# Kernel tuning notes

Measured on AMD Instinct MI355X. Metric: run time of the kernel, lower is better.

Reference implementation:

```python
import jax, jax.numpy as jnp
import numpy as np

N = 100000          # number of nodes (src == dst in this sampled graph)
DEG = 8             # uniform sampled fan-in (max_num_neighbors)
E = N * DEG         # number of edges
IN_C = 128
HEADS = 4
OUT_C = 32
NEG_SLOPE = 0.2


def setup_inputs() -> dict:
    key = jax.random.key(0)
    k1, k2, k3, k4, k5 = jax.random.split(key, 5)
    x = jax.random.normal(k1, (N, IN_C), dtype=jnp.float32)
    csr_row_ptr = jnp.arange(N + 1, dtype=jnp.int64) * DEG
    csr_col_ind = jax.random.randint(k2, (E,), 0, N, dtype=jnp.int64)
    # learned params (xavier-normal-ish scaling)
    lin_w = jax.random.normal(k3, (IN_C, HEADS * OUT_C), dtype=jnp.float32) * np.sqrt(2.0 / (IN_C + HEADS * OUT_C))
    att = jax.random.normal(k4, (2 * HEADS * OUT_C,), dtype=jnp.float32) * np.sqrt(2.0 / (1 + OUT_C))
    bias = jnp.zeros((HEADS * OUT_C,), dtype=jnp.float32)
    return {"x": x, "csr_row_ptr": csr_row_ptr, "csr_col_ind": csr_col_ind,
            "max_num_neighbors": DEG, "lin_w": lin_w, "att": att, "bias": bias}


def reference(x, csr_row_ptr, csr_col_ind, max_num_neighbors, lin_w, att, bias):
    n = x.shape[0]
    e = csr_col_ind.shape[0]
    hc = HEADS * OUT_C
    # linear projection: [N, H, C]
    xp = (x @ lin_w).reshape(n, HEADS, OUT_C)
    att_src = att[:hc].reshape(HEADS, OUT_C)
    att_dst = att[hc:].reshape(HEADS, OUT_C)
    # per-node attention logits per head: [N, H]
    a_src = jnp.einsum('nhc,hc->nh', xp, att_src)
    a_dst = jnp.einsum('nhc,hc->nh', xp, att_dst)
    # expand CSR row_ptr into per-edge destination ids: [E]
    dst = jnp.searchsorted(csr_row_ptr, jnp.arange(e, dtype=csr_row_ptr.dtype), side='right') - 1
    src = csr_col_ind
    # edge scores + per-destination softmax over incoming edges
    logits = jax.nn.leaky_relu(a_src[src] + a_dst[dst], NEG_SLOPE)  # [E, H]
    m = jax.ops.segment_max(logits, dst, num_segments=n)            # [N, H]
    ex = jnp.exp(logits - m[dst])
    denom = jax.ops.segment_sum(ex, dst, num_segments=n)            # [N, H]
    alpha = ex / denom[dst]                                         # [E, H]
    # weighted aggregation of neighbor features: [N, H, C]
    out = jax.ops.segment_sum(alpha[:, :, None] * xp[src], dst, num_segments=n)
    out = out.reshape(n, hc) + bias  # concat=True
    return out
```

## Files before the change

kernel.cpp:

```cpp
#include <hip/hip_runtime.h>
#include <stdint.h>

#define HEADS 4
#define NEG_SLOPE 0.2f
#define MB 64

typedef _Float16 f16;
typedef f16 f16x8 __attribute__((ext_vector_type(8)));
typedef f16 f16x4 __attribute__((ext_vector_type(4)));
typedef float f32x4 __attribute__((ext_vector_type(4)));
typedef unsigned int u32x4 __attribute__((ext_vector_type(4)));

#define SWZ(row, kb) (((row) << 8) + ((kb) ^ (((row) & 7) << 4)))

__global__ __launch_bounds__(256) void wt_kernel(const float* __restrict__ w,
                                                 f16* __restrict__ wt) {
    __shared__ f16 tl[16][136];
    const int b = blockIdx.x, t = threadIdx.x;
    for (int i = t; i < 2048; i += 256) {
        int k = i >> 4, nl = i & 15;
        tl[nl][k] = (f16)w[k * 128 + b * 16 + nl];
    }
    __syncthreads();
    {
        int nl = t >> 4, kc = t & 15;
        f16x8 v = *(const f16x8*)&tl[nl][kc * 8];
        *(f16x8*)(wt + (b * 16 + nl) * 128 + kc * 8) = v;
    }
}

__global__ __launch_bounds__(256) void gat_proj_mfma(
    const float* __restrict__ x, const f16* __restrict__ wt,
    const float* __restrict__ att, f16* __restrict__ xp,
    float* __restrict__ a_src, float* __restrict__ a_dst, int n) {
    __shared__ unsigned char lds[32768];
    __shared__ float att_l[256];
    const int t = threadIdx.x;
    const int node0 = blockIdx.x * MB;
    const int lane = t & 63;
    const int wv = t >> 6;

    att_l[t] = att[t];

    const int arow = node0 + wv * 16 + (lane & 15);
    const bool rowok = arow < n;
    const float* xr = x + (size_t)arow * 128 + (lane >> 4) * 8;
    f16x8 afr[4];
#pragma unroll
    for (int kt = 0; kt < 4; kt++) {
        float4 a = make_float4(0.f, 0.f, 0.f, 0.f), b = a;
        if (rowok) {
            a = *(const float4*)(xr + kt * 32);
            b = *(const float4*)(xr + kt * 32 + 4);
        }
        f16x8 hv;
        hv[0] = (f16)a.x; hv[1] = (f16)a.y; hv[2] = (f16)a.z; hv[3] = (f16)a.w;
        hv[4] = (f16)b.x; hv[5] = (f16)b.y; hv[6] = (f16)b.z; hv[7] = (f16)b.w;
        afr[kt] = hv;
    }

    for (int i = t; i < 2048; i += 256) {
        int row = i >> 4, kc = i & 15;
        uint4 v = *(const uint4*)(wt + row * 128 + kc * 8);
        *(uint4*)(lds + SWZ(row, kc * 16)) = v;
    }
    __syncthreads();

    f32x4 acc[8];
#pragma unroll
    for (int nf = 0; nf < 8; nf++) acc[nf] = (f32x4){0.f, 0.f, 0.f, 0.f};

#pragma unroll
    for (int kt = 0; kt < 4; kt++) {
        const int kb = kt * 64 + (lane >> 4) * 16;
#pragma unroll
        for (int nf = 0; nf < 8; nf++) {
            f16x8 bfr = *(const f16x8*)(lds + SWZ(nf * 16 + (lane & 15), kb));
            acc[nf] = __builtin_amdgcn_mfma_f32_16x16x32_f16(afr[kt], bfr, acc[nf], 0, 0, 0);
        }
    }

    __syncthreads();
#pragma unroll
    for (int r = 0; r < 4; r++) {
        int row = wv * 16 + (lane >> 4) * 4 + r;
#pragma unroll
        for (int nf = 0; nf < 8; nf++) {
            int col = nf * 16 + (lane & 15);
            *(f16*)(lds + SWZ(row, col * 2)) = (f16)acc[nf][r];
        }
    }
    __syncthreads();

    {
        int row = t >> 2, h = t & 3;
        int grow = node0 + row;
        if (grow < n) {
            float s = 0.f, d = 0.f;
#pragma unroll
            for (int cc = 0; cc < 4; cc++) {
                f16x8 v = *(const f16x8*)(lds + SWZ(row, h * 64 + cc * 16));
#pragma unroll
                for (int j = 0; j < 8; j++) {
                    float xv = (float)v[j];
                    int c = cc * 8 + j;
                    s = fmaf(xv, att_l[h * 32 + c], s);
                    d = fmaf(xv, att_l[128 + h * 32 + c], d);
                }
            }
            a_src[(size_t)grow * HEADS + h] = s;
            a_dst[(size_t)grow * HEADS + h] = d;
        }
    }
    for (int i = t; i < 1024; i += 256) {
        int row = i >> 4, kc = i & 15;
        int grow = node0 + row;
        if (grow < n) {
            u32x4 v = *(const u32x4*)(lds + SWZ(row, kc * 16));
            int slice = kc >> 2;
            *(u32x4*)(xp + ((size_t)slice * n + grow) * 32 + (kc & 3) * 8) = v;
        }
    }
}

__global__ __launch_bounds__(256) void gat_alpha_kernel(
    const float* __restrict__ a_src, const float* __restrict__ a_dst,
    const int* __restrict__ row_ptr, const int* __restrict__ col_ind,
    f16* __restrict__ alpha, int n, int e_total) {
    const int lane = threadIdx.x & 63;
    const int nb = (blockIdx.x * 4 + (threadIdx.x >> 6)) * 8;
    if (nb >= n) return;
    const int j = lane >> 3, e = lane & 7;
    const int node = nb + j;

    int rp = 0;
    if (lane < 9) {
        int idx = nb + lane;
        if (idx > n) idx = n;
        rp = row_ptr[idx];
    }
    bool ok = __all((lane < 9) ? (rp == (nb + lane) * 8) : 1) && (nb + 8 <= n);

    int ci = 0;
    bool valid;
    if (ok) {
        ci = col_ind[nb * 8 + lane];
        valid = true;
    } else {
        int rs = __shfl(rp, j, 64), re = __shfl(rp, j + 1, 64);
        int dg = re - rs;
        if (dg > 8) dg = 8;
        valid = (node < n) && (e < dg);
        if (valid) ci = col_ind[rs + e];
    }

    f32x4 asv = (f32x4){0.f, 0.f, 0.f, 0.f};
    if (valid) asv = *(const f32x4*)(a_src + (size_t)ci * HEADS);
    f32x4 adv = (f32x4){0.f, 0.f, 0.f, 0.f};
    if (node < n) adv = *(const f32x4*)(a_dst + (size_t)node * HEADS);

#pragma unroll
    for (int h = 0; h < HEADS; h++) {
        float z = asv[h] + adv[h];
        z = (z >= 0.f) ? z : NEG_SLOPE * z;
        float v = valid ? z : -1e30f;
        float m = v;
        m = fmaxf(m, __shfl_xor(m, 1, 64));
        m = fmaxf(m, __shfl_xor(m, 2, 64));
        m = fmaxf(m, __shfl_xor(m, 4, 64));
        float ex = valid ? __expf(v - m) : 0.f;
        float ss = ex;
        ss += __shfl_xor(ss, 1, 64);
        ss += __shfl_xor(ss, 2, 64);
        ss += __shfl_xor(ss, 4, 64);
        float al = ex * ((ss > 0.f) ? (1.f / ss) : 0.f);
        if (node < n)
            alpha[(size_t)h * n * 8 + (size_t)node * 8 + e] = (f16)al;
    }
}

__global__ __launch_bounds__(256) void gat_slice_aggr(
    const f16* __restrict__ xp, const f16* __restrict__ alpha,
    const int* __restrict__ row_ptr, const int* __restrict__ col_ind,
    const float* __restrict__ bias, float* __restrict__ out, int n, int e_total) {
    const int slice = blockIdx.x & 3;
    const int chunk = blockIdx.x >> 2;
    const int lane = threadIdx.x & 63;
    const int nb = chunk * 32 + (threadIdx.x >> 6) * 8;
    if (nb >= n) return;

    const f16* xps = xp + (size_t)slice * n * 32;
    const f16* alp = alpha + (size_t)slice * n * 8;
    const int nd = lane >> 3, c = lane & 7;
    const int node = nb + nd;

    int rp = 0;
    if (lane < 9) {
        int idx = nb + lane;
        if (idx > n) idx = n;
        rp = row_ptr[idx];
    }
    int ci = 0;
    {
        long long si = (long long)nb * 8 + lane;
        if (si < e_total) ci = col_ind[si];
    }
    int av = 0;
    if (lane < 32) {
        long long fi = (long long)nb * 8 + lane * 2;
        if (fi + 2 <= (long long)n * 8) av = *(const int*)(alp + fi);
    }
    float4 b4 = *(const float4*)(bias + slice * 32 + c * 4);

    bool ok = __all((lane < 9) ? (rp == (nb + lane) * 8) : 1) && (nb + 8 <= n);

    float a0 = 0.f, a1 = 0.f, a2 = 0.f, a3 = 0.f;
    if (ok) {
#pragma unroll
        for (int e = 0; e < 8; e++) {
            int src = __shfl(ci, nd * 8 + e, 64);
            int au = __shfl(av, (nd * 8 + e) >> 1, 64);
            unsigned short ab = (e & 1) ? (unsigned short)(((unsigned int)au) >> 16)
                                        : (unsigned short)(au & 0xffff);
            float a = (float)(*(const f16*)&ab);
            f16x4 v = *(const f16x4*)(xps + (size_t)src * 32 + c * 4);
            a0 = fmaf(a, (float)v[0], a0);
            a1 = fmaf(a, (float)v[1], a1);
            a2 = fmaf(a, (float)v[2], a2);
            a3 = fmaf(a, (float)v[3], a3);
        }
    } else {
        int rs = __shfl(rp, nd, 64);
        int re = __shfl(rp, nd + 1, 64);
        int dg = re - rs;
        if (dg > 8) dg = 8;
        if (node < n) {
            for (int e = 0; e < dg; e++) {
                int src = col_ind[rs + e];
                unsigned short ab = *(const unsigned short*)(alp + (size_t)node * 8 + e);
                float a = (float)(*(const f16*)&ab);
                f16x4 v = *(const f16x4*)(xps + (size_t)src * 32 + c * 4);
                a0 = fmaf(a, (float)v[0], a0);
                a1 = fmaf(a, (float)v[1], a1);
                a2 = fmaf(a, (float)v[2], a2);
                a3 = fmaf(a, (float)v[3], a3);
            }
        }
    }

    if (node < n) {
        f32x4 o;
        o[0] = a0 + b4.x;
        o[1] = a1 + b4.y;
        o[2] = a2 + b4.z;
        o[3] = a3 + b4.w;
        __builtin_nontemporal_store(o, (f32x4*)(out + (size_t)node * 128 + slice * 32 + c * 4));
    }
}

extern "C" void kernel_launch(void* const* d_in, const int* in_sizes, int n_in,
                              void* d_out, int out_size, void* d_ws, size_t ws_size,
                              hipStream_t stream) {
    const float* x = (const float*)d_in[0];
    const int* row_ptr = (const int*)d_in[1];
    const int* col_ind = (const int*)d_in[2];
    const float* lin_w = (const float*)d_in[4];
    const float* att = (const float*)d_in[5];
    const float* bias = (const float*)d_in[6];
    float* out = (float*)d_out;
    const int n = in_sizes[0] / 128;
    const int e_total = in_sizes[2];

    f16* xp = (f16*)d_ws;
    float* a_src = (float*)((char*)d_ws + (size_t)n * 256);
    float* a_dst = a_src + (size_t)n * HEADS;
    f16* alpha = (f16*)(a_dst + (size_t)n * HEADS);
    f16* wt = alpha + (size_t)n * 32 + 128;

    hipLaunchKernelGGL(wt_kernel, dim3(8), dim3(256), 0, stream, lin_w, wt);
    hipLaunchKernelGGL(gat_proj_mfma, dim3((n + MB - 1) / MB), dim3(256), 0, stream,
                       x, wt, att, xp, a_src, a_dst, n);
    hipLaunchKernelGGL(gat_alpha_kernel, dim3((n + 31) / 32), dim3(256), 0, stream,
                       a_src, a_dst, row_ptr, col_ind, alpha, n, e_total);
    hipLaunchKernelGGL(gat_slice_aggr, dim3(4 * ((n + 31) / 32)), dim3(256), 0, stream,
                       xp, alpha, row_ptr, col_ind, bias, out, n, e_total);
}
```

Baseline: 75.35 us.

## Fuse edge softmax into slice aggregation kernel and drop alpha buffer

Removes the separate alpha kernel. Each aggregation wavefront now computes the leaky-relu logits, segment max and softmax for its own head slice using warp shuffles, reading a_src and a_dst directly. This drops one launch and the alpha write and read round trip through memory. The eight neighbor feature gathers are now issued before the softmax math so they can overlap with it, at the cost of more registers and scattered a_src gathers repeated once per slice.

```diff
diff --git a/kernel.cpp b/kernel.cpp
--- a/kernel.cpp
+++ b/kernel.cpp
@@ -123,15 +123,20 @@
     }
 }
 
-__global__ __launch_bounds__(256) void gat_alpha_kernel(
-    const float* __restrict__ a_src, const float* __restrict__ a_dst,
-    const int* __restrict__ row_ptr, const int* __restrict__ col_ind,
-    f16* __restrict__ alpha, int n, int e_total) {
+__global__ __launch_bounds__(256) void gat_slice_aggr(
+    const f16* __restrict__ xp, const float* __restrict__ a_src,
+    const float* __restrict__ a_dst, const int* __restrict__ row_ptr,
+    const int* __restrict__ col_ind, const float* __restrict__ bias,
+    float* __restrict__ out, int n, int e_total) {
+    const int slice = blockIdx.x & 3;
+    const int chunk = blockIdx.x >> 2;
     const int lane = threadIdx.x & 63;
-    const int nb = (blockIdx.x * 4 + (threadIdx.x >> 6)) * 8;
+    const int nb = chunk * 32 + (threadIdx.x >> 6) * 8;
     if (nb >= n) return;
-    const int j = lane >> 3, e = lane & 7;
-    const int node = nb + j;
+
+    const f16* xps = xp + (size_t)slice * n * 32;
+    const int nd = lane >> 3, x8 = lane & 7;
+    const int node = nb + nd;
 
     int rp = 0;
     if (lane < 9) {
@@ -139,113 +144,55 @@
         if (idx > n) idx = n;
         rp = row_ptr[idx];
     }
-    bool ok = __all((lane < 9) ? (rp == (nb + lane) * 8) : 1) && (nb + 8 <= n);
-
-    int ci = 0;
-    bool valid;
-    if (ok) {
-        ci = col_ind[nb * 8 + lane];
-        valid = true;
-    } else {
-        int rs = __shfl(rp, j, 64), re = __shfl(rp, j + 1, 64);
-        int dg = re - rs;
-        if (dg > 8) dg = 8;
-        valid = (node < n) && (e < dg);
-        if (valid) ci = col_ind[rs + e];
-    }
-
-    f32x4 asv = (f32x4){0.f, 0.f, 0.f, 0.f};
-    if (valid) asv = *(const f32x4*)(a_src + (size_t)ci * HEADS);
-    f32x4 adv = (f32x4){0.f, 0.f, 0.f, 0.f};
-    if (node < n) adv = *(const f32x4*)(a_dst + (size_t)node * HEADS);
-
-#pragma unroll
-    for (int h = 0; h < HEADS; h++) {
-        float z = asv[h] + adv[h];
-        z = (z >= 0.f) ? z : NEG_SLOPE * z;
-        float v = valid ? z : -1e30f;
-        float m = v;
-        m = fmaxf(m, __shfl_xor(m, 1, 64));
-        m = fmaxf(m, __shfl_xor(m, 2, 64));
-        m = fmaxf(m, __shfl_xor(m, 4, 64));
-        float ex = valid ? __expf(v - m) : 0.f;
-        float ss = ex;
-        ss += __shfl_xor(ss, 1, 64);
-        ss += __shfl_xor(ss, 2, 64);
-        ss += __shfl_xor(ss, 4, 64);
-        float al = ex * ((ss > 0.f) ? (1.f / ss) : 0.f);
-        if (node < n)
-            alpha[(size_t)h * n * 8 + (size_t)node * 8 + e] = (f16)al;
-    }
-}
-
-__global__ __launch_bounds__(256) void gat_slice_aggr(
-    const f16* __restrict__ xp, const f16* __restrict__ alpha,
-    const int* __restrict__ row_ptr, const int* __restrict__ col_ind,
-    const float* __restrict__ bias, float* __restrict__ out, int n, int e_total) {
-    const int slice = blockIdx.x & 3;
-    const int chunk = blockIdx.x >> 2;
-    const int lane = threadIdx.x & 63;
-    const int nb = chunk * 32 + (threadIdx.x >> 6) * 8;
-    if (nb >= n) return;
-
-    const f16* xps = xp + (size_t)slice * n * 32;
-    const f16* alp = alpha + (size_t)slice * n * 8;
-    const int nd = lane >> 3, c = lane & 7;
-    const int node = nb + nd;
-
-    int rp = 0;
-    if (lane < 9) {
-        int idx = nb + lane;
-        if (idx > n) idx = n;
-        rp = row_ptr[idx];
-    }
     int ci = 0;
     {
         long long si = (long long)nb * 8 + lane;
         if (si < e_total) ci = col_ind[si];
     }
-    int av = 0;
-    if (lane < 32) {
-        long long fi = (long long)nb * 8 + lane * 2;
-        if (fi + 2 <= (long long)n * 8) av = *(const int*)(alp + fi);
-    }
-    float4 b4 = *(const float4*)(bias + slice * 32 + c * 4);
+    float4 b4 = *(const float4*)(bias + slice * 32 + x8 * 4);
 
     bool ok = __all((lane < 9) ? (rp == (nb + lane) * 8) : 1) && (nb + 8 <= n);
-
-    float a0 = 0.f, a1 = 0.f, a2 = 0.f, a3 = 0.f;
-    if (ok) {
-#pragma unroll
-        for (int e = 0; e < 8; e++) {
-            int src = __shfl(ci, nd * 8 + e, 64);
-            int au = __shfl(av, (nd * 8 + e) >> 1, 64);
-            unsigned short ab = (e & 1) ? (unsigned short)(((unsigned int)au) >> 16)
-                                        : (unsigned short)(au & 0xffff);
-            float a = (float)(*(const f16*)&ab);
-            f16x4 v = *(const f16x4*)(xps + (size_t)src * 32 + c * 4);
-            a0 = fmaf(a, (float)v[0], a0);
-            a1 = fmaf(a, (float)v[1], a1);
-            a2 = fmaf(a, (float)v[2], a2);
-            a3 = fmaf(a, (float)v[3], a3);
-        }
-    } else {
-        int rs = __shfl(rp, nd, 64);
-        int re = __shfl(rp, nd + 1, 64);
+    bool valid = true;
+    if (!ok) {
+        int rs = __shfl(rp, nd, 64), re = __shfl(rp, nd + 1, 64);
         int dg = re - rs;
         if (dg > 8) dg = 8;
-        if (node < n) {
-            for (int e = 0; e < dg; e++) {
-                int src = col_ind[rs + e];
-                unsigned short ab = *(const unsigned short*)(alp + (size_t)node * 8 + e);
-                float a = (float)(*(const f16*)&ab);
-                f16x4 v = *(const f16x4*)(xps + (size_t)src * 32 + c * 4);
-                a0 = fmaf(a, (float)v[0], a0);
-                a1 = fmaf(a, (float)v[1], a1);
-                a2 = fmaf(a, (float)v[2], a2);
-                a3 = fmaf(a, (float)v[3], a3);
-            }
-        }
+        if (node >= n) dg = 0;
+        valid = x8 < dg;
+        ci = valid ? col_ind[rs + x8] : 0;
+    }
+
+    f16x4 pv[8];
+#pragma unroll
+    for (int e = 0; e < 8; e++) {
+        int src = __shfl(ci, nd * 8 + e, 64);
+        pv[e] = *(const f16x4*)(xps + (size_t)src * 32 + x8 * 4);
+    }
+
+    float as = valid ? a_src[(size_t)ci * HEADS + slice] : 0.f;
+    float ad = (node < n) ? a_dst[(size_t)node * HEADS + slice] : 0.f;
+    float z = as + ad;
+    z = (z >= 0.f) ? z : NEG_SLOPE * z;
+    float v = valid ? z : -1e30f;
+    float m = v;
+    m = fmaxf(m, __shfl_xor(m, 1, 64));
+    m = fmaxf(m, __shfl_xor(m, 2, 64));
+    m = fmaxf(m, __shfl_xor(m, 4, 64));
+    float ex = valid ? __expf(v - m) : 0.f;
+    float ss = ex;
+    ss += __shfl_xor(ss, 1, 64);
+    ss += __shfl_xor(ss, 2, 64);
+    ss += __shfl_xor(ss, 4, 64);
+    float alpha = ex * ((ss > 0.f) ? (1.f / ss) : 0.f);
+
+    float a0 = 0.f, a1 = 0.f, a2 = 0.f, a3 = 0.f;
+#pragma unroll
+    for (int e = 0; e < 8; e++) {
+        float a = __shfl(alpha, nd * 8 + e, 64);
+        a0 = fmaf(a, (float)pv[e][0], a0);
+        a1 = fmaf(a, (float)pv[e][1], a1);
+        a2 = fmaf(a, (float)pv[e][2], a2);
+        a3 = fmaf(a, (float)pv[e][3], a3);
     }
 
     if (node < n) {
@@ -254,7 +201,7 @@
         o[1] = a1 + b4.y;
         o[2] = a2 + b4.z;
         o[3] = a3 + b4.w;
-        __builtin_nontemporal_store(o, (f32x4*)(out + (size_t)node * 128 + slice * 32 + c * 4));
+        __builtin_nontemporal_store(o, (f32x4*)(out + (size_t)node * 128 + slice * 32 + x8 * 4));
     }
 }
 
@@ -274,14 +221,11 @@
     f16* xp = (f16*)d_ws;
     float* a_src = (float*)((char*)d_ws + (size_t)n * 256);
     float* a_dst = a_src + (size_t)n * HEADS;
-    f16* alpha = (f16*)(a_dst + (size_t)n * HEADS);
-    f16* wt = alpha + (size_t)n * 32 + 128;
+    f16* wt = (f16*)(a_dst + (size_t)n * HEADS);
 
     hipLaunchKernelGGL(wt_kernel, dim3(8), dim3(256), 0, stream, lin_w, wt);
     hipLaunchKernelGGL(gat_proj_mfma, dim3((n + MB - 1) / MB), dim3(256), 0, stream,
                        x, wt, att, xp, a_src, a_dst, n);
-    hipLaunchKernelGGL(gat_alpha_kernel, dim3((n + 31) / 32), dim3(256), 0, stream,
-                       a_src, a_dst, row_ptr, col_ind, alpha, n, e_total);
     hipLaunchKernelGGL(gat_slice_aggr, dim3(4 * ((n + 31) / 32)), dim3(256), 0, stream,
-                       xp, alpha, row_ptr, col_ind, bias, out, n, e_total);
-}
+                       xp, a_src, a_dst, row_ptr, col_ind, bias, out, n, e_total);
+}
```

Result: slower. 83.79 us (+11.2%).
